# Optimization experiments

Measured on AMD Instinct MI355X. Metric: run time of the kernel, lower is better.

Reference implementation:

```python
import jax, jax.numpy as jnp
import numpy as np

DIM = 1024
NUM_HEADS = 16
HEAD_DIM = DIM // NUM_HEADS
GATE_HID = DIM // 4


def setup_inputs() -> dict:
    key = jax.random.key(0)
    ks = jax.random.split(key, 16)
    B, S, D = 2, 2048, DIM
    sc = 1.0 / np.sqrt(D)
    inp = {
        "h": jax.random.normal(ks[0], (B, S, D), jnp.float32),
        "x": jax.random.normal(ks[1], (B, S, D), jnp.float32),
        # attention projections, stored (in, out) so y = x @ W + b
        "Wq": jax.random.normal(ks[2], (D, D), jnp.float32) * sc,
        "bq": jnp.zeros((D,), jnp.float32),
        "Wk": jax.random.normal(ks[3], (D, D), jnp.float32) * sc,
        "bk": jnp.zeros((D,), jnp.float32),
        "Wv": jax.random.normal(ks[4], (D, D), jnp.float32) * sc,
        "bv": jnp.zeros((D,), jnp.float32),
        "Wo": jax.random.normal(ks[5], (D, D), jnp.float32) * sc,
        "bo": jnp.zeros((D,), jnp.float32),
        # gating MLP: Linear(2D -> D//4) -> GELU -> Linear(D//4 -> D) -> sigmoid
        "Wg1": jax.random.normal(ks[6], (2 * D, GATE_HID), jnp.float32) * (1.0 / np.sqrt(2 * D)),
        "bg1": jnp.zeros((GATE_HID,), jnp.float32),
        "Wg2": jax.random.normal(ks[7], (GATE_HID, D), jnp.float32) * (1.0 / np.sqrt(GATE_HID)),
        "bg2": jnp.zeros((D,), jnp.float32),
    }
    return inp


def reference(h, x, Wq, bq, Wk, bk, Wv, bv, Wo, bo, Wg1, bg1, Wg2, bg2):
    B, S, D = h.shape
    # gated blend of latent h and input x
    gate_in = jnp.concatenate([h, x], axis=-1)                      # (B,S,2D)
    gate = jax.nn.sigmoid((jax.nn.gelu(gate_in @ Wg1 + bg1, approximate=False)) @ Wg2 + bg2)
    blended = gate * h + (1.0 - gate) * x                           # (B,S,D)
    # multi-head self-attention
    q = (blended @ Wq + bq).reshape(B, S, NUM_HEADS, HEAD_DIM)
    k = (blended @ Wk + bk).reshape(B, S, NUM_HEADS, HEAD_DIM)
    v = (blended @ Wv + bv).reshape(B, S, NUM_HEADS, HEAD_DIM)
    scale = 1.0 / np.sqrt(HEAD_DIM).astype(np.float32)
    scores = jnp.einsum('bqhd,bkhd->bhqk', q, k) * scale            # (B,H,S,S)
    attn = jax.nn.softmax(scores, axis=-1)
    out = jnp.einsum('bhqk,bkhd->bqhd', attn, v).reshape(B, S, D)
    return out @ Wo + bo
```

## Files before the change

### kernel.cpp

```cpp
#include <hip/hip_runtime.h>
#include <hip/hip_bf16.h>


typedef __attribute__((ext_vector_type(4))) unsigned int u32x4;
typedef __attribute__((ext_vector_type(2))) unsigned int u32x2;
typedef __attribute__((ext_vector_type(8))) short s16x8;
typedef __attribute__((ext_vector_type(8))) unsigned short u16x8;
typedef __attribute__((ext_vector_type(4))) float f32x4;

#define QSCALE 0.18033688011112043f
#define FIXED_M 24.0f

__device__ __forceinline__ unsigned short f2bf(float f) {
    unsigned int i = __builtin_bit_cast(unsigned int, f) + 0x8000u;
    return (unsigned short)(i >> 16);
}
__device__ __forceinline__ unsigned int pack2bf(float a, float b) {
    unsigned int ia = __builtin_bit_cast(unsigned int, a) + 0x8000u;
    unsigned int ib = __builtin_bit_cast(unsigned int, b) + 0x8000u;
    return __builtin_amdgcn_perm(ib, ia, 0x07060302u);
}

__device__ __forceinline__ void gload16(const void* g, void* l) {
    __builtin_amdgcn_global_load_lds(
        (const __attribute__((address_space(1))) void*)g,
        (__attribute__((address_space(3))) void*)l, 16, 0, 0);
}

struct TEntry { const float* src; unsigned short* dst; int K; int N; };
struct TTable { TEntry e[6]; };

__global__ __launch_bounds__(256) void prep_all(
    TTable tt,
    const float* __restrict__ h, const float* __restrict__ x,
    unsigned short* __restrict__ hx,
    const float* __restrict__ bq, const float* __restrict__ bk,
    const float* __restrict__ bv, float* __restrict__ bqkv)
{
    const int bid = (int)blockIdx.x;
    const int tid = threadIdx.x;
    if (bid < 3072) {
        const TEntry E = tt.e[bid >> 9];
        const int bx = bid & 511;
        const int ntn = E.N >> 5;
        if (bx >= (E.K >> 6) * ntn) return;
        const int n0 = (bx % ntn) * 32, k0 = (bx / ntn) * 64;
        __shared__ float tile[64][33];
        const int lnn = tid & 31, lkk = tid >> 5;
#pragma unroll
        for (int i = 0; i < 8; ++i)
            tile[lkk + i * 8][lnn] = E.src[(size_t)(k0 + lkk + i * 8) * E.N + n0 + lnn];
        __syncthreads();
        const int snn = tid >> 3, skk = (tid & 7) * 8;
        u16x8 o;
#pragma unroll
        for (int j = 0; j < 8; ++j) o[j] = f2bf(tile[skk + j][snn]);
        *reinterpret_cast<u16x8*>(&E.dst[(size_t)(n0 + snn) * E.K + k0 + skk]) = o;
        return;
    }
    if (bid < 3072 + 4096) {
        const int idx = (bid - 3072) * 256 + tid;
        const size_t e = (size_t)idx * 8;
        const int r = (int)(e >> 11), c = (int)(e & 2047);
        const float* src = (c < 1024) ? (h + (size_t)r * 1024 + c)
                                      : (x + (size_t)r * 1024 + (c - 1024));
        u16x8 o;
#pragma unroll
        for (int j = 0; j < 8; ++j) o[j] = f2bf(src[j]);
        *reinterpret_cast<u16x8*>(hx + e) = o;
        return;
    }
    const int i = (bid - 3072 - 4096) * 256 + tid;
    if (i < 1024) bqkv[i] = bq[i];
    else if (i < 2048) bqkv[i] = bk[i - 1024];
    else if (i < 3072) bqkv[i] = bv[i - 2048];
}

__global__ __launch_bounds__(256) void transpose_v(
    const unsigned short* __restrict__ qkv, unsigned short* __restrict__ vt)
{
    __shared__ unsigned short t[64][65];
    const int st = blockIdx.x;
    const int bh = blockIdx.y;
    const int b = bh >> 4, h = bh & 15;
    const int tx = threadIdx.x & 63, ty = threadIdx.x >> 6;
    const int s0 = st * 64;
    const size_t base = (size_t)(b * 2048 + s0) * 3072 + 2048 + h * 64;
#pragma unroll
    for (int i = 0; i < 16; ++i)
        t[ty + i * 4][tx] = qkv[base + (size_t)(ty + i * 4) * 3072 + tx];
    __syncthreads();
    const size_t obase = (size_t)(bh * 64) * 2048 + s0;
#pragma unroll
    for (int i = 0; i < 16; ++i)
        vt[obase + (size_t)(ty + i * 4) * 2048 + tx] = t[tx][ty + i * 4];
}

enum { EPI_GELU = 1, EPI_BLEND = 2, EPI_F32 = 3, EPI_QKV = 4 };

template <int EPI>
__global__ __launch_bounds__(256, 3) void gemm_kernel(
    const unsigned short* __restrict__ A, int lda,
    const unsigned short* __restrict__ Bt, int ldb,
    const float* __restrict__ bias,
    void* __restrict__ Cv, int ldc, int K,
    const float* __restrict__ hb, const float* __restrict__ xb,
    int swzn, int ntn)
{
    __shared__ unsigned short Alds[2][128 * 32];
    __shared__ unsigned short Blds[2][128 * 32];

    const int tid = threadIdx.x;
    const int lane = tid & 63;
    const int w = tid >> 6;
    const int wr = w >> 1, wc = w & 1;
    int mt, nt;
    if (swzn > 0) {
        const int xcd = (int)blockIdx.x & 7, seq = (int)blockIdx.x >> 3;
        nt = xcd * swzn + seq % swzn;
        mt = seq / swzn;
    } else {
        nt = (int)blockIdx.x % ntn;
        mt = (int)blockIdx.x / ntn;
    }
    const int m0 = mt * 128, n0 = nt * 128;
    const int lrow = lane & 15, lko = (lane >> 4) * 8;

    const int grow = w * 32 + (lane >> 2);
    const int gk8 = (lane & 3) * 8;
    const unsigned short* ga0 = A + (size_t)(m0 + grow) * lda + gk8;
    const unsigned short* ga1 = ga0 + (size_t)16 * lda;
    const unsigned short* gb0 = Bt + (size_t)(n0 + grow) * ldb + gk8;
    const unsigned short* gb1 = gb0 + (size_t)16 * ldb;

    auto stage = [&](int buf, int k0) {
        unsigned short* la = &Alds[buf][w * 1024];
        unsigned short* lb = &Blds[buf][w * 1024];
        gload16(ga0 + k0, la);
        gload16(ga1 + k0, la + 512);
        gload16(gb0 + k0, lb);
        gload16(gb1 + k0, lb + 512);
    };

    f32x4 acc[4][4];
#pragma unroll
    for (int i = 0; i < 4; ++i)
#pragma unroll
        for (int j = 0; j < 4; ++j) acc[i][j] = (f32x4){0.f, 0.f, 0.f, 0.f};

    const int kks = K >> 5;
    stage(0, 0);
    __syncthreads();

    for (int t = 0; t < kks; ++t) {
        const int cur = t & 1;
        if (t + 1 < kks) stage(cur ^ 1, (t + 1) << 5);

        s16x8 af[4], bfr[4];
#pragma unroll
        for (int mi = 0; mi < 4; ++mi)
            af[mi] = *reinterpret_cast<const s16x8*>(&Alds[cur][(wr * 64 + mi * 16 + lrow) * 32 + lko]);
#pragma unroll
        for (int ni = 0; ni < 4; ++ni)
            bfr[ni] = *reinterpret_cast<const s16x8*>(&Blds[cur][(wc * 64 + ni * 16 + lrow) * 32 + lko]);
#pragma unroll
        for (int mi = 0; mi < 4; ++mi)
#pragma unroll
            for (int ni = 0; ni < 4; ++ni)
                acc[mi][ni] = __builtin_amdgcn_mfma_f32_16x16x32_bf16(af[mi], bfr[ni], acc[mi][ni], 0, 0, 0);

        __syncthreads();
    }

    const int rbase = m0 + wr * 64;
    const int cbase = n0 + wc * 64;
#pragma unroll
    for (int mi = 0; mi < 4; ++mi) {
#pragma unroll
        for (int j = 0; j < 4; ++j) {
            const int r = rbase + mi * 16 + (lane >> 4) * 4 + j;
#pragma unroll
            for (int ni = 0; ni < 4; ++ni) {
                const int c = cbase + ni * 16 + (lane & 15);
                float v = acc[mi][ni][j] + bias[c];
                if constexpr (EPI == EPI_GELU) {
                    float g = 0.5f * v * (1.f + erff(v * 0.70710678118654752f));
                    ((unsigned short*)Cv)[(size_t)r * ldc + c] = f2bf(g);
                } else if constexpr (EPI == EPI_BLEND) {
                    float gate = 1.f / (1.f + __expf(-v));
                    const size_t o = (size_t)r * ldc + c;
                    float bl = gate * hb[o] + (1.f - gate) * xb[o];
                    ((unsigned short*)Cv)[o] = f2bf(bl);
                } else if constexpr (EPI == EPI_QKV) {
                    const float scl = (c < 1024) ? QSCALE : 1.f;
                    ((unsigned short*)Cv)[(size_t)r * ldc + c] = f2bf(v * scl);
                } else {
                    ((float*)Cv)[(size_t)r * ldc + c] = v;
                }
            }
        }
    }
}

template <int EPI>
__global__ __launch_bounds__(256, 4) void gemm64_kernel(
    const unsigned short* __restrict__ A, int lda,
    const unsigned short* __restrict__ Bt, int ldb,
    const float* __restrict__ bias,
    void* __restrict__ Cv, int ldc, int K,
    const float* __restrict__ hb, const float* __restrict__ xb,
    int swzn)
{
    __shared__ unsigned short Alds[2][64 * 32];
    __shared__ unsigned short Blds[2][64 * 32];

    const int tid = threadIdx.x;
    const int lane = tid & 63;
    const int w = tid >> 6;
    const int wr = w >> 1, wc = w & 1;
    const int xcd = (int)blockIdx.x & 7, seq = (int)blockIdx.x >> 3;
    const int nt = xcd * swzn + seq % swzn;
    const int mt = seq / swzn;
    const int m0 = mt * 64, n0 = nt * 64;
    const int lrow = lane & 15, lko = (lane >> 4) * 8;

    const int grow = w * 16 + (lane >> 2);
    const int gk8 = (lane & 3) * 8;
    const unsigned short* ga = A + (size_t)(m0 + grow) * lda + gk8;
    const unsigned short* gb = Bt + (size_t)(n0 + grow) * ldb + gk8;

    auto stage = [&](int buf, int k0) {
        gload16(ga + k0, &Alds[buf][w * 512]);
        gload16(gb + k0, &Blds[buf][w * 512]);
    };

    f32x4 acc[2][2];
#pragma unroll
    for (int i = 0; i < 2; ++i)
#pragma unroll
        for (int j = 0; j < 2; ++j) acc[i][j] = (f32x4){0.f, 0.f, 0.f, 0.f};

    const int kks = K >> 5;
    stage(0, 0);
    __syncthreads();

    for (int t = 0; t < kks; ++t) {
        const int cur = t & 1;
        if (t + 1 < kks) stage(cur ^ 1, (t + 1) << 5);

        s16x8 af[2], bfr[2];
#pragma unroll
        for (int mi = 0; mi < 2; ++mi)
            af[mi] = *reinterpret_cast<const s16x8*>(&Alds[cur][(wr * 32 + mi * 16 + lrow) * 32 + lko]);
#pragma unroll
        for (int ni = 0; ni < 2; ++ni)
            bfr[ni] = *reinterpret_cast<const s16x8*>(&Blds[cur][(wc * 32 + ni * 16 + lrow) * 32 + lko]);
#pragma unroll
        for (int mi = 0; mi < 2; ++mi)
#pragma unroll
            for (int ni = 0; ni < 2; ++ni)
                acc[mi][ni] = __builtin_amdgcn_mfma_f32_16x16x32_bf16(af[mi], bfr[ni], acc[mi][ni], 0, 0, 0);

        __syncthreads();
    }

    const int rbase = m0 + wr * 32;
    const int cbase = n0 + wc * 32;
#pragma unroll
    for (int mi = 0; mi < 2; ++mi) {
#pragma unroll
        for (int j = 0; j < 4; ++j) {
            const int r = rbase + mi * 16 + (lane >> 4) * 4 + j;
#pragma unroll
            for (int ni = 0; ni < 2; ++ni) {
                const int c = cbase + ni * 16 + (lane & 15);
                float v = acc[mi][ni][j] + bias[c];
                if constexpr (EPI == EPI_BLEND) {
                    float gate = 1.f / (1.f + __expf(-v));
                    const size_t o = (size_t)r * ldc + c;
                    float bl = gate * hb[o] + (1.f - gate) * xb[o];
                    ((unsigned short*)Cv)[o] = f2bf(bl);
                } else {
                    ((float*)Cv)[(size_t)r * ldc + c] = v;
                }
            }
        }
    }
}

__global__ __launch_bounds__(256, 2) void gemm_gelu64(
    const unsigned short* __restrict__ A, int lda,
    const unsigned short* __restrict__ Bt, int ldb,
    const float* __restrict__ bias,
    unsigned short* __restrict__ C, int ldc, int K)
{
    __shared__ unsigned short Alds[2][64 * 32];
    __shared__ unsigned short Blds[2][64 * 32];

    const int tid = threadIdx.x;
    const int lane = tid & 63;
    const int w = tid >> 6;
    const int wr = w >> 1, wc = w & 1;
    const int nt = (int)blockIdx.x & 3, mt = (int)blockIdx.x >> 2;
    const int m0 = mt * 64, n0 = nt * 64;
    const int lrow = lane & 15, lko = (lane >> 4) * 8;

    const int grow = w * 16 + (lane >> 2);
    const int gk8 = (lane & 3) * 8;
    const unsigned short* ga = A + (size_t)(m0 + grow) * lda + gk8;
    const unsigned short* gb = Bt + (size_t)(n0 + grow) * ldb + gk8;

    auto stage = [&](int buf, int k0) {
        gload16(ga + k0, &Alds[buf][w * 512]);
        gload16(gb + k0, &Blds[buf][w * 512]);
    };

    f32x4 acc[2][2];
#pragma unroll
    for (int i = 0; i < 2; ++i)
#pragma unroll
        for (int j = 0; j < 2; ++j) acc[i][j] = (f32x4){0.f, 0.f, 0.f, 0.f};

    const int kks = K >> 5;
    stage(0, 0);
    __syncthreads();

    for (int t = 0; t < kks; ++t) {
        const int cur = t & 1;
        if (t + 1 < kks) stage(cur ^ 1, (t + 1) << 5);

        s16x8 af[2], bfr[2];
#pragma unroll
        for (int mi = 0; mi < 2; ++mi)
            af[mi] = *reinterpret_cast<const s16x8*>(&Alds[cur][(wr * 32 + mi * 16 + lrow) * 32 + lko]);
#pragma unroll
        for (int ni = 0; ni < 2; ++ni)
            bfr[ni] = *reinterpret_cast<const s16x8*>(&Blds[cur][(wc * 32 + ni * 16 + lrow) * 32 + lko]);
#pragma unroll
        for (int mi = 0; mi < 2; ++mi)
#pragma unroll
            for (int ni = 0; ni < 2; ++ni)
                acc[mi][ni] = __builtin_amdgcn_mfma_f32_16x16x32_bf16(af[mi], bfr[ni], acc[mi][ni], 0, 0, 0);

        __syncthreads();
    }

    const int rbase = m0 + wr * 32;
    const int cbase = n0 + wc * 32;
#pragma unroll
    for (int mi = 0; mi < 2; ++mi) {
#pragma unroll
        for (int j = 0; j < 4; ++j) {
            const int r = rbase + mi * 16 + (lane >> 4) * 4 + j;
#pragma unroll
            for (int ni = 0; ni < 2; ++ni) {
                const int c = cbase + ni * 16 + (lane & 15);
                float v = acc[mi][ni][j] + bias[c];
                float g = 0.5f * v * (1.f + erff(v * 0.70710678118654752f));
                C[(size_t)r * ldc + c] = f2bf(g);
            }
        }
    }
}

#define ALD 72

__global__ __launch_bounds__(256, 4) void attn_kernel(
    const unsigned short* __restrict__ qkv,
    const unsigned short* __restrict__ vt,
    unsigned short* __restrict__ out)
{
    __shared__ unsigned short Klds[2][64 * 64];
    __shared__ unsigned short Vlds[2][64 * 64];
    __shared__ unsigned short Plds[4][16 * ALD];

    const int tid = threadIdx.x, lane = tid & 63, w = tid >> 6;
    const int xcd = (int)blockIdx.x & 7, seq = (int)blockIdx.x >> 3;
    const int bh = xcd * 4 + (seq & 3);
    const int qt = seq >> 2;
    const int b = bh >> 4, h = bh & 15;
    const int rb = b * 2048;
    const int lrow = lane & 15, g = lane >> 4, lko = g * 8;

    s16x8 qf[2][2];
#pragma unroll
    for (int qg = 0; qg < 2; ++qg) {
        const size_t qrow = (size_t)(rb + qt * 128 + w * 32 + qg * 16 + lrow) * 3072 + h * 64;
        qf[qg][0] = *reinterpret_cast<const s16x8*>(qkv + qrow + lko);
        qf[qg][1] = *reinterpret_cast<const s16x8*>(qkv + qrow + 32 + lko);
    }

    const int grow = w * 16 + (lane >> 3);
    const int gswz = ((lane & 7) ^ (lane >> 3)) * 8;
    const unsigned short* kgp = qkv + (size_t)(rb + grow) * 3072 + 1024 + h * 64 + gswz;
    const unsigned short* vgp = vt + (size_t)(bh * 64 + grow) * 2048 + gswz;

    auto stage = [&](int buf, int t0) {
        gload16(kgp + (size_t)t0 * 3072, &Klds[buf][w * 1024]);
        gload16(kgp + (size_t)(t0 + 8) * 3072, &Klds[buf][w * 1024 + 512]);
        gload16(vgp + t0, &Vlds[buf][w * 1024]);
        gload16(vgp + t0 + 8 * 2048, &Vlds[buf][w * 1024 + 512]);
    };

    const int cs0 = ((g) ^ (lrow & 7)) * 8;
    const int cs1 = ((4 + g) ^ (lrow & 7)) * 8;

    f32x4 acc0[4], acc1[4];
#pragma unroll
    for (int di = 0; di < 4; ++di) {
        acc0[di] = (f32x4){0.f, 0.f, 0.f, 0.f};
        acc1[di] = (f32x4){0.f, 0.f, 0.f, 0.f};
    }
    float lsum0 = 0.f, lsum1 = 0.f;

    unsigned short* pw = &Plds[w][0];

    stage(0, 0);
    __syncthreads();

    for (int t0 = 0; t0 < 2048; t0 += 64) {
        const int cur = (t0 >> 6) & 1;
        if (t0 + 64 < 2048) stage(cur ^ 1, t0 + 64);

        s16x8 kf[4][2];
#pragma unroll
        for (int ni = 0; ni < 4; ++ni) {
            kf[ni][0] = *reinterpret_cast<const s16x8*>(&Klds[cur][(ni * 16 + lrow) * 64 + cs0]);
            kf[ni][1] = *reinterpret_cast<const s16x8*>(&Klds[cur][(ni * 16 + lrow) * 64 + cs1]);
        }

        f32x4 s0[4];
#pragma unroll
        for (int ni = 0; ni < 4; ++ni) s0[ni] = (f32x4){0.f, 0.f, 0.f, 0.f};
#pragma unroll
        for (int ni = 0; ni < 4; ++ni)
#pragma unroll
            for (int fi = 0; fi < 2; ++fi)
                s0[ni] = __builtin_amdgcn_mfma_f32_16x16x32_bf16(kf[ni][fi], qf[0][fi], s0[ni], 0, 0, 0);

#pragma unroll
        for (int ni = 0; ni < 4; ++ni) {
            float p0 = __builtin_amdgcn_exp2f(s0[ni][0] - FIXED_M);
            float p1 = __builtin_amdgcn_exp2f(s0[ni][1] - FIXED_M);
            float p2 = __builtin_amdgcn_exp2f(s0[ni][2] - FIXED_M);
            float p3 = __builtin_amdgcn_exp2f(s0[ni][3] - FIXED_M);
            lsum0 += (p0 + p1) + (p2 + p3);
            u32x2 pk = {pack2bf(p0, p1), pack2bf(p2, p3)};
            *reinterpret_cast<u32x2*>(&pw[lrow * ALD + ni * 16 + g * 4]) = pk;
        }

        f32x4 s1[4];
#pragma unroll
        for (int ni = 0; ni < 4; ++ni) s1[ni] = (f32x4){0.f, 0.f, 0.f, 0.f};
#pragma unroll
        for (int ni = 0; ni < 4; ++ni)
#pragma unroll
            for (int fi = 0; fi < 2; ++fi)
                s1[ni] = __builtin_amdgcn_mfma_f32_16x16x32_bf16(kf[ni][fi], qf[1][fi], s1[ni], 0, 0, 0);

        s16x8 vf[2][4];
#pragma unroll
        for (int di = 0; di < 4; ++di) {
            vf[0][di] = *reinterpret_cast<const s16x8*>(&Vlds[cur][(di * 16 + lrow) * 64 + cs0]);
            vf[1][di] = *reinterpret_cast<const s16x8*>(&Vlds[cur][(di * 16 + lrow) * 64 + cs1]);
        }

#pragma unroll
        for (int st = 0; st < 2; ++st) {
            s16x8 pf = *reinterpret_cast<const s16x8*>(&pw[lrow * ALD + st * 32 + lko]);
#pragma unroll
            for (int di = 0; di < 4; ++di)
                acc0[di] = __builtin_amdgcn_mfma_f32_16x16x32_bf16(vf[st][di], pf, acc0[di], 0, 0, 0);
        }

#pragma unroll
        for (int ni = 0; ni < 4; ++ni) {
            float p0 = __builtin_amdgcn_exp2f(s1[ni][0] - FIXED_M);
            float p1 = __builtin_amdgcn_exp2f(s1[ni][1] - FIXED_M);
            float p2 = __builtin_amdgcn_exp2f(s1[ni][2] - FIXED_M);
            float p3 = __builtin_amdgcn_exp2f(s1[ni][3] - FIXED_M);
            lsum1 += (p0 + p1) + (p2 + p3);
            u32x2 pk = {pack2bf(p0, p1), pack2bf(p2, p3)};
            *reinterpret_cast<u32x2*>(&pw[lrow * ALD + ni * 16 + g * 4]) = pk;
        }

#pragma unroll
        for (int st = 0; st < 2; ++st) {
            s16x8 pf = *reinterpret_cast<const s16x8*>(&pw[lrow * ALD + st * 32 + lko]);
#pragma unroll
            for (int di = 0; di < 4; ++di)
                acc1[di] = __builtin_amdgcn_mfma_f32_16x16x32_bf16(vf[st][di], pf, acc1[di], 0, 0, 0);
        }

        __syncthreads();
    }

    lsum0 += __shfl_xor(lsum0, 16);
    lsum0 += __shfl_xor(lsum0, 32);
    lsum1 += __shfl_xor(lsum1, 16);
    lsum1 += __shfl_xor(lsum1, 32);
    const float inv0 = 1.f / lsum0;
    const float inv1 = 1.f / lsum1;
    const size_t orow0 = (size_t)(rb + qt * 128 + w * 32 + lrow) * 1024 + h * 64;
    const size_t orow1 = orow0 + (size_t)16 * 1024;
#pragma unroll
    for (int di = 0; di < 4; ++di) {
        u32x2 ov0 = {pack2bf(acc0[di][0] * inv0, acc0[di][1] * inv0),
                     pack2bf(acc0[di][2] * inv0, acc0[di][3] * inv0)};
        *reinterpret_cast<u32x2*>(&out[orow0 + di * 16 + g * 4]) = ov0;
        u32x2 ov1 = {pack2bf(acc1[di][0] * inv1, acc1[di][1] * inv1),
                     pack2bf(acc1[di][2] * inv1, acc1[di][3] * inv1)};
        *reinterpret_cast<u32x2*>(&out[orow1 + di * 16 + g * 4]) = ov1;
    }
}

extern "C" void kernel_launch(void* const* d_in, const int* in_sizes, int n_in,
                              void* d_out, int out_size, void* d_ws, size_t ws_size,
                              hipStream_t stream)
{
    const float* h   = (const float*)d_in[0];
    const float* x   = (const float*)d_in[1];
    const float* Wq  = (const float*)d_in[2];
    const float* bq  = (const float*)d_in[3];
    const float* Wk  = (const float*)d_in[4];
    const float* bk  = (const float*)d_in[5];
    const float* Wv  = (const float*)d_in[6];
    const float* bv  = (const float*)d_in[7];
    const float* Wo  = (const float*)d_in[8];
    const float* bo  = (const float*)d_in[9];
    const float* Wg1 = (const float*)d_in[10];
    const float* bg1 = (const float*)d_in[11];
    const float* Wg2 = (const float*)d_in[12];
    const float* bg2 = (const float*)d_in[13];

    char* ws = (char*)d_ws;
    size_t off = 0;
    auto alloc = [&](size_t bytes) {
        void* p = ws + off;
        off += (bytes + 255) & ~(size_t)255;
        return p;
    };
    unsigned short* wg1T  = (unsigned short*)alloc((size_t)256 * 2048 * 2);
    unsigned short* wg2T  = (unsigned short*)alloc((size_t)1024 * 256 * 2);
    unsigned short* wqkvT = (unsigned short*)alloc((size_t)3072 * 1024 * 2);
    unsigned short* woT   = (unsigned short*)alloc((size_t)1024 * 1024 * 2);
    float*          bqkv  = (float*)alloc((size_t)3072 * 4);
    unsigned short* blend = (unsigned short*)alloc((size_t)4096 * 1024 * 2);
    unsigned short* attno = (unsigned short*)alloc((size_t)4096 * 1024 * 2);
    unsigned short* vtb   = (unsigned short*)alloc((size_t)32 * 64 * 2048 * 2);
    char* uni = (char*)alloc((size_t)4096 * 3072 * 2);
    unsigned short* hx  = (unsigned short*)uni;
    unsigned short* g1  = (unsigned short*)(uni + (size_t)4096 * 2048 * 2);
    unsigned short* qkv = (unsigned short*)uni;
    (void)ws_size; (void)in_sizes; (void)n_in; (void)out_size;

    TTable tt;
    tt.e[0] = {Wg1, wg1T, 2048, 256};
    tt.e[1] = {Wg2, wg2T, 256, 1024};
    tt.e[2] = {Wq, wqkvT, 1024, 1024};
    tt.e[3] = {Wk, wqkvT + (size_t)1024 * 1024, 1024, 1024};
    tt.e[4] = {Wv, wqkvT + (size_t)2048 * 1024, 1024, 1024};
    tt.e[5] = {Wo, woT, 1024, 1024};
    prep_all<<<3072 + 4096 + 12, 256, 0, stream>>>(tt, h, x, hx, bq, bk, bv, bqkv);

    gemm_gelu64<<<256, 256, 0, stream>>>(hx, 2048, wg1T, 2048, bg1, g1, 256, 2048);
    gemm64_kernel<EPI_BLEND><<<1024, 256, 0, stream>>>(
        g1, 256, wg2T, 256, bg2, blend, 1024, 256, h, x, 2);

    gemm_kernel<EPI_QKV><<<768, 256, 0, stream>>>(
        blend, 1024, wqkvT, 1024, bqkv, qkv, 3072, 1024, nullptr, nullptr, 3, 24);

    transpose_v<<<dim3(32, 32), 256, 0, stream>>>(qkv, vtb);

    attn_kernel<<<512, 256, 0, stream>>>(qkv, vtb, attno);

    gemm64_kernel<EPI_F32><<<1024, 256, 0, stream>>>(
        attno, 1024, woT, 1024, bo, (float*)d_out, 1024, 1024, nullptr, nullptr, 2);
}
```

Measured before the change: 166.0 us.

## Fuse h/x bf16 conversion into gate GEMM and software-pipeline attention PV

The separate pass that converts h and x into a concatenated bf16 buffer is removed. The gate GEMM now reads the fp32 rows directly into registers, converts them, and writes them to LDS after the MFMAs, so the intermediate write and read of the hx buffer disappear. In the attention kernel, the P·V MFMAs for each tile are deferred to the next iteration so they overlap with the next QK computation, and the occupancy hint is lowered from 4 to 3 blocks to allow more registers. The trade-offs are register-staged A loads in place of async global-to-LDS loads, and lower attention occupancy.

```diff
diff --git a/kernel.cpp b/kernel.cpp
--- a/kernel.cpp
+++ b/kernel.cpp
@@ -32,8 +32,6 @@
 
 __global__ __launch_bounds__(256) void prep_all(
     TTable tt,
-    const float* __restrict__ h, const float* __restrict__ x,
-    unsigned short* __restrict__ hx,
     const float* __restrict__ bq, const float* __restrict__ bk,
     const float* __restrict__ bv, float* __restrict__ bqkv)
 {
@@ -58,19 +56,7 @@
         *reinterpret_cast<u16x8*>(&E.dst[(size_t)(n0 + snn) * E.K + k0 + skk]) = o;
         return;
     }
-    if (bid < 3072 + 4096) {
-        const int idx = (bid - 3072) * 256 + tid;
-        const size_t e = (size_t)idx * 8;
-        const int r = (int)(e >> 11), c = (int)(e & 2047);
-        const float* src = (c < 1024) ? (h + (size_t)r * 1024 + c)
-                                      : (x + (size_t)r * 1024 + (c - 1024));
-        u16x8 o;
-#pragma unroll
-        for (int j = 0; j < 8; ++j) o[j] = f2bf(src[j]);
-        *reinterpret_cast<u16x8*>(hx + e) = o;
-        return;
-    }
-    const int i = (bid - 3072 - 4096) * 256 + tid;
+    const int i = (bid - 3072) * 256 + tid;
     if (i < 1024) bqkv[i] = bq[i];
     else if (i < 2048) bqkv[i] = bk[i - 1024];
     else if (i < 3072) bqkv[i] = bv[i - 2048];
@@ -289,7 +275,7 @@
 }
 
 __global__ __launch_bounds__(256, 2) void gemm_gelu64(
-    const unsigned short* __restrict__ A, int lda,
+    const float* __restrict__ h, const float* __restrict__ x,
     const unsigned short* __restrict__ Bt, int ldb,
     const float* __restrict__ bias,
     unsigned short* __restrict__ C, int ldc, int K)
@@ -307,13 +293,19 @@
 
     const int grow = w * 16 + (lane >> 2);
     const int gk8 = (lane & 3) * 8;
-    const unsigned short* ga = A + (size_t)(m0 + grow) * lda + gk8;
     const unsigned short* gb = Bt + (size_t)(n0 + grow) * ldb + gk8;
-
-    auto stage = [&](int buf, int k0) {
-        gload16(ga + k0, &Alds[buf][w * 512]);
-        gload16(gb + k0, &Blds[buf][w * 512]);
+    const size_t arow = (size_t)(m0 + grow) * 1024;
+
+    auto loadA = [&](int k0, f32x4& lo, f32x4& hi) {
+        const float* src = (k0 < 1024 ? h : x) + arow + (k0 & 1023) + gk8;
+        lo = *reinterpret_cast<const f32x4*>(src);
+        hi = *reinterpret_cast<const f32x4*>(src + 4);
     };
+    auto writeA = [&](int buf, const f32x4& lo, const f32x4& hi) {
+        u32x4 p = {pack2bf(lo[0], lo[1]), pack2bf(lo[2], lo[3]),
+                   pack2bf(hi[0], hi[1]), pack2bf(hi[2], hi[3])};
+        *reinterpret_cast<u32x4*>(&Alds[buf][grow * 32 + gk8]) = p;
+    };
 
     f32x4 acc[2][2];
 #pragma unroll
@@ -322,12 +314,18 @@
         for (int j = 0; j < 2; ++j) acc[i][j] = (f32x4){0.f, 0.f, 0.f, 0.f};
 
     const int kks = K >> 5;
-    stage(0, 0);
+    f32x4 alo, ahi;
+    loadA(0, alo, ahi);
+    gload16(gb, &Blds[0][w * 512]);
+    writeA(0, alo, ahi);
     __syncthreads();
 
     for (int t = 0; t < kks; ++t) {
         const int cur = t & 1;
-        if (t + 1 < kks) stage(cur ^ 1, (t + 1) << 5);
+        if (t + 1 < kks) {
+            loadA((t + 1) << 5, alo, ahi);
+            gload16(gb + ((t + 1) << 5), &Blds[cur ^ 1][w * 512]);
+        }
 
         s16x8 af[2], bfr[2];
 #pragma unroll
@@ -342,6 +340,7 @@
             for (int ni = 0; ni < 2; ++ni)
                 acc[mi][ni] = __builtin_amdgcn_mfma_f32_16x16x32_bf16(af[mi], bfr[ni], acc[mi][ni], 0, 0, 0);
 
+        if (t + 1 < kks) writeA(cur ^ 1, alo, ahi);
         __syncthreads();
     }
 
@@ -365,7 +364,7 @@
 
 #define ALD 72
 
-__global__ __launch_bounds__(256, 4) void attn_kernel(
+__global__ __launch_bounds__(256, 3) void attn_kernel(
     const unsigned short* __restrict__ qkv,
     const unsigned short* __restrict__ vt,
     unsigned short* __restrict__ out)
@@ -414,6 +413,7 @@
     float lsum0 = 0.f, lsum1 = 0.f;
 
     unsigned short* pw = &Plds[w][0];
+    s16x8 vf[2][4];
 
     stage(0, 0);
     __syncthreads();
@@ -421,6 +421,16 @@
     for (int t0 = 0; t0 < 2048; t0 += 64) {
         const int cur = (t0 >> 6) & 1;
         if (t0 + 64 < 2048) stage(cur ^ 1, t0 + 64);
+
+        if (t0 > 0) {
+#pragma unroll
+            for (int st = 0; st < 2; ++st) {
+                s16x8 pf = *reinterpret_cast<const s16x8*>(&pw[lrow * ALD + st * 32 + lko]);
+#pragma unroll
+                for (int di = 0; di < 4; ++di)
+                    acc1[di] = __builtin_amdgcn_mfma_f32_16x16x32_bf16(vf[st][di], pf, acc1[di], 0, 0, 0);
+            }
+        }
 
         s16x8 kf[4][2];
 #pragma unroll
@@ -458,7 +468,6 @@
             for (int fi = 0; fi < 2; ++fi)
                 s1[ni] = __builtin_amdgcn_mfma_f32_16x16x32_bf16(kf[ni][fi], qf[1][fi], s1[ni], 0, 0, 0);
 
-        s16x8 vf[2][4];
 #pragma unroll
         for (int di = 0; di < 4; ++di) {
             vf[0][di] = *reinterpret_cast<const s16x8*>(&Vlds[cur][(di * 16 + lrow) * 64 + cs0]);
@@ -484,15 +493,15 @@
             *reinterpret_cast<u32x2*>(&pw[lrow * ALD + ni * 16 + g * 4]) = pk;
         }
 
-#pragma unroll
-        for (int st = 0; st < 2; ++st) {
-            s16x8 pf = *reinterpret_cast<const s16x8*>(&pw[lrow * ALD + st * 32 + lko]);
-#pragma unroll
-            for (int di = 0; di < 4; ++di)
-                acc1[di] = __builtin_amdgcn_mfma_f32_16x16x32_bf16(vf[st][di], pf, acc1[di], 0, 0, 0);
-        }
-
         __syncthreads();
+    }
+
+#pragma unroll
+    for (int st = 0; st < 2; ++st) {
+        s16x8 pf = *reinterpret_cast<const s16x8*>(&pw[lrow * ALD + st * 32 + lko]);
+#pragma unroll
+        for (int di = 0; di < 4; ++di)
+            acc1[di] = __builtin_amdgcn_mfma_f32_16x16x32_bf16(vf[st][di], pf, acc1[di], 0, 0, 0);
     }
 
     lsum0 += __shfl_xor(lsum0, 16);
@@ -548,10 +557,8 @@
     unsigned short* blend = (unsigned short*)alloc((size_t)4096 * 1024 * 2);
     unsigned short* attno = (unsigned short*)alloc((size_t)4096 * 1024 * 2);
     unsigned short* vtb   = (unsigned short*)alloc((size_t)32 * 64 * 2048 * 2);
-    char* uni = (char*)alloc((size_t)4096 * 3072 * 2);
-    unsigned short* hx  = (unsigned short*)uni;
-    unsigned short* g1  = (unsigned short*)(uni + (size_t)4096 * 2048 * 2);
-    unsigned short* qkv = (unsigned short*)uni;
+    unsigned short* g1    = (unsigned short*)alloc((size_t)4096 * 256 * 2);
+    unsigned short* qkv   = (unsigned short*)alloc((size_t)4096 * 3072 * 2);
     (void)ws_size; (void)in_sizes; (void)n_in; (void)out_size;
 
     TTable tt;
@@ -561,9 +568,9 @@
     tt.e[3] = {Wk, wqkvT + (size_t)1024 * 1024, 1024, 1024};
     tt.e[4] = {Wv, wqkvT + (size_t)2048 * 1024, 1024, 1024};
     tt.e[5] = {Wo, woT, 1024, 1024};
-    prep_all<<<3072 + 4096 + 12, 256, 0, stream>>>(tt, h, x, hx, bq, bk, bv, bqkv);
-
-    gemm_gelu64<<<256, 256, 0, stream>>>(hx, 2048, wg1T, 2048, bg1, g1, 256, 2048);
+    prep_all<<<3072 + 12, 256, 0, stream>>>(tt, bq, bk, bv, bqkv);
+
+    gemm_gelu64<<<256, 256, 0, stream>>>(h, x, wg1T, 2048, bg1, g1, 256, 2048);
     gemm64_kernel<EPI_BLEND><<<1024, 256, 0, stream>>>(
         g1, 256, wg2T, 256, bg2, blend, 1024, 256, h, x, 2);
 
```

Measured after the change: 164.9 us. Within noise of the previous version (-0.6%).
